# Performance work log

Measured on AMD Instinct MI355X. Metric: run time of the kernel, lower is better.

The kernel has to match this reference:

```python
import math
import jax, jax.numpy as jnp
import numpy as np

SIZE = 8
STEEPNESS = 10.0
BATCH = 262144


def setup_inputs() -> dict:
    key = jax.random.key(0)
    k1, k2 = jax.random.split(key)
    pred_scores = jax.random.normal(k1, (BATCH, SIZE), dtype=jnp.float32)
    labels = jax.random.normal(k2, (BATCH, SIZE), dtype=jnp.float32)
    rank_ema = jnp.zeros((SIZE,), dtype=jnp.float32)  # fresh-module EMA buffer
    return {"pred_scores": pred_scores, "labels": labels, "rank_ema": rank_ema}


def _odd_even_diffsort(x, steepness=STEEPNESS):
    """Differentiable odd-even sorting network (cauchy distribution).
    x: [B, n]. Returns (sorted_values [B, n], perm [B, n, n]) with
    x @ perm == sorted_values (perm tracks columns, matching diffsort)."""
    B, n = x.shape
    P = jnp.broadcast_to(jnp.eye(n, dtype=x.dtype), (B, n, n))
    for layer in range(n):  # odd-even network has n layers for size n
        start = layer % 2
        idx_a = np.arange(start, n - 1, 2)  # static indices
        idx_b = idx_a + 1
        a = x[:, idx_a]
        b = x[:, idx_b]
        # Cauchy CDF of (b - a): alpha -> 1 when pair already sorted (a < b)
        alpha = jnp.arctan(steepness * (b - a)) / math.pi + 0.5  # [B, k]
        new_a = alpha * a + (1.0 - alpha) * b          # soft min -> lower index
        new_b = (1.0 - alpha) * a + alpha * b          # soft max -> upper index
        x = x.at[:, idx_a].set(new_a).at[:, idx_b].set(new_b)
        colA = P[:, :, idx_a]  # [B, n, k]
        colB = P[:, :, idx_b]
        al = alpha[:, None, :]
        P = P.at[:, :, idx_a].set(al * colA + (1.0 - al) * colB)
        P = P.at[:, :, idx_b].set((1.0 - al) * colA + al * colB)
    return x, P


def reference(pred_scores, labels, rank_ema):
    n = pred_scores.shape[-1]
    rank_indices = jnp.argsort(-labels, axis=-1)          # [B, n]
    rank_true = jnp.argsort(rank_indices, axis=-1)        # inverse permutation
    select_rank_ema = rank_ema[rank_true]                 # [B, n]
    shifted = pred_scores - select_rank_ema
    # (EMA buffer update is a detached side effect; it does not affect the loss)
    _, perm_prediction = _odd_even_diffsort(-shifted)
    # one_hot(argsort(-labels)).transpose(-2, -1)
    perm_ground_truth = jnp.swapaxes(jax.nn.one_hot(rank_indices, n, dtype=jnp.float32), -2, -1)
    p = perm_prediction.astype(jnp.float32)
    # torch BCELoss clamps each log term at -100
    log_p = jnp.clip(jnp.log(p), -100.0, None)
    log_1mp = jnp.clip(jnp.log1p(-p), -100.0, None)
    ce_loss = -jnp.mean(perm_ground_truth * log_p + (1.0 - perm_ground_truth) * log_1mp)
    return ce_loss
```

## Files before the change

### kernel.cpp

```cpp
#include <hip/hip_runtime.h>
#include <math.h>

#define BATCH 262144
#define N 8
#define BLK 64
#define NBLK (BATCH / BLK)
#define NCMP 28

typedef float v2f __attribute__((ext_vector_type(2)));

struct Net { int a[NCMP]; unsigned sup2[N / 2][NCMP]; };
constexpr Net make_net() {
    Net n{};
    int k = 0;
    for (int L = 0; L < N; ++L)
        for (int a = (L & 1); a < N - 1; a += 2)
            n.a[k++] = a;
    for (int r = 0; r < N / 2; ++r) {
        unsigned s = (1u << (2 * r)) | (1u << (2 * r + 1));
        for (int q = 0; q < NCMP; ++q) {
            n.sup2[r][q] = s;
            unsigned m = 3u << n.a[q];
            if (s & m) s |= m;
        }
    }
    return n;
}
constexpr Net NET = make_net();

__device__ __forceinline__ float cauchy_alpha(float z10) {
    float az  = __builtin_fabsf(z10);
    bool  big = az > 1.0f;
    float inv = __builtin_amdgcn_rcpf(az);
    float t   = big ? inv : az;
    float t2  = t * t;
    float p   = 0.1417796f;
    p = __builtin_fmaf(p, t2, -0.3258092f);
    p = __builtin_fmaf(p, t2, 0.9992150f);
    float at = p * t;
    float r  = big ? (1.5707963267948966f - at) : at;
    float sr = __builtin_copysignf(r, z10);
    return __builtin_fmaf(sr, 0.31830988618379067f, 0.5f);
}

__global__ __launch_bounds__(BLK, 4) void diffsort_loss_kernel(
    const float* __restrict__ pred,
    const float* __restrict__ labels,
    const float* __restrict__ rank_ema,
    float* __restrict__ partial)
{
    const int row = blockIdx.x * BLK + threadIdx.x;

    __shared__ float ema[N];
    if (threadIdx.x < N) ema[threadIdx.x] = rank_ema[threadIdx.x];
    __syncthreads();

    const float4* lp = (const float4*)(labels + (size_t)row * N);
    const float4* pp = (const float4*)(pred   + (size_t)row * N);
    float4 l0 = lp[0], l1 = lp[1];
    float4 p0 = pp[0], p1 = pp[1];
    float lab[N] = {l0.x, l0.y, l0.z, l0.w, l1.x, l1.y, l1.z, l1.w};
    float prd[N] = {p0.x, p0.y, p0.z, p0.w, p1.x, p1.y, p1.z, p1.w};

    int rt[N];
#pragma unroll
    for (int i = 0; i < N; ++i) rt[i] = 0;
#pragma unroll
    for (int i = 0; i < N; ++i)
#pragma unroll
        for (int j = i + 1; j < N; ++j) {
            unsigned c = lab[j] > lab[i];
            rt[i] += c;
            rt[j] += 1u - c;
        }

    float x[N];
#pragma unroll
    for (int i = 0; i < N; ++i)
        x[i] = ema[rt[i]] - prd[i];

    v2f p2[N / 2][N];
#pragma unroll
    for (int r = 0; r < N / 2; ++r)
#pragma unroll
        for (int j = 0; j < N; ++j) {
            v2f v;
            v.x = (j == 2 * r)     ? 1.0f : 0.0f;
            v.y = (j == 2 * r + 1) ? 1.0f : 0.0f;
            p2[r][j] = v;
        }

#pragma unroll
    for (int k = 0; k < NCMP; ++k) {
        const int ia = NET.a[k], ib = ia + 1;
        const float a = x[ia], b = x[ib];
        const float z = b - a;
        const float alpha = cauchy_alpha(10.0f * z);
        x[ia] = __builtin_fmaf(-alpha, z, b);
        x[ib] = __builtin_fmaf( alpha, z, a);
        v2f al2; al2.x = alpha; al2.y = alpha;
#pragma unroll
        for (int r = 0; r < N / 2; ++r) {
            const bool live = ((NET.sup2[r][k] >> ia) | (NET.sup2[r][k] >> ib)) & 1u;
            if (live) {
                const v2f ca = p2[r][ia], cb = p2[r][ib];
                const v2f d  = ca - cb;
                p2[r][ia] = __builtin_elementwise_fma( al2, d, cb);
                p2[r][ib] = __builtin_elementwise_fma(-al2, d, ca);
            }
        }
    }

    float s = 0.0f;
#pragma unroll
    for (int r = 0; r < N / 2; ++r) {
        const int h0 = rt[2 * r], h1 = rt[2 * r + 1];
        v2f arg; arg.x = 1.0f; arg.y = 1.0f;
#pragma unroll
        for (int j = 0; j < N; ++j) {
            const v2f pv = p2[r][j];
            v2f one; one.x = 1.0f; one.y = 1.0f;
            const v2f qv = one - pv;
            v2f f;
            f.x = (h0 == j) ? pv.x : qv.x;
            f.y = (h1 == j) ? pv.y : qv.y;
            arg *= f;
        }
        s += __logf(fmaxf(arg.x, 1e-37f));
        s += __logf(fmaxf(arg.y, 1e-37f));
    }

#pragma unroll
    for (int off = 32; off > 0; off >>= 1)
        s += __shfl_down(s, off);
    if (threadIdx.x == 0) partial[blockIdx.x] = s;
}

__global__ __launch_bounds__(256) void reduce_partials(
    const float* __restrict__ partial, float* __restrict__ out)
{
    float s = 0.0f;
#pragma unroll
    for (int k = 0; k < NBLK / 256; ++k)
        s += partial[threadIdx.x + k * 256];
#pragma unroll
    for (int off = 32; off > 0; off >>= 1)
        s += __shfl_down(s, off);

    __shared__ float wsum[4];
    const int lane = threadIdx.x & 63;
    const int wid  = threadIdx.x >> 6;
    if (lane == 0) wsum[wid] = s;
    __syncthreads();
    if (threadIdx.x == 0) {
        const float tot = wsum[0] + wsum[1] + wsum[2] + wsum[3];
        out[0] = -tot * (1.0f / 16777216.0f);
    }
}

extern "C" void kernel_launch(void* const* d_in, const int* in_sizes, int n_in,
                              void* d_out, int out_size, void* d_ws, size_t ws_size,
                              hipStream_t stream)
{
    const float* pred     = (const float*)d_in[0];
    const float* labels   = (const float*)d_in[1];
    const float* rank_ema = (const float*)d_in[2];
    float* out     = (float*)d_out;
    float* partial = (float*)d_ws;

    diffsort_loss_kernel<<<NBLK, BLK, 0, stream>>>(pred, labels, rank_ema, partial);
    reduce_partials<<<1, 256, 0, stream>>>(partial, out);
}
```

Baseline: 77.53 us.

## Split each row across two threads, each tracking half the permutation rows

Each batch row is now handled by two threads. Both recompute the label ranks and the sort-value network, and each propagates four of the eight permutation rows, initialised via a lane-dependent select. This doubles thread count and halves per-thread permutation state and register pressure, but duplicates the loads, rank computation and alpha arctan chain. The static liveness pruning of dead permutation entries is removed, so some zero updates are now computed, and the occupancy hint on launch bounds is dropped.

New measurement: 81.65 us. 5.3% more time.

```diff
diff --git a/kernel.cpp b/kernel.cpp
--- a/kernel.cpp
+++ b/kernel.cpp
@@ -4,29 +4,19 @@
 #define BATCH 262144
 #define N 8
 #define BLK 64
-#define NBLK (BATCH / BLK)
+#define ROWS_PER_BLK 32
+#define NBLK (BATCH / ROWS_PER_BLK)
 #define NCMP 28
 
 typedef float v2f __attribute__((ext_vector_type(2)));
 
-struct Net { int a[NCMP]; unsigned sup2[N / 2][NCMP]; };
-constexpr Net make_net() {
-    Net n{};
-    int k = 0;
+constexpr int cmp_a(int k) {
+    int q = 0;
     for (int L = 0; L < N; ++L)
         for (int a = (L & 1); a < N - 1; a += 2)
-            n.a[k++] = a;
-    for (int r = 0; r < N / 2; ++r) {
-        unsigned s = (1u << (2 * r)) | (1u << (2 * r + 1));
-        for (int q = 0; q < NCMP; ++q) {
-            n.sup2[r][q] = s;
-            unsigned m = 3u << n.a[q];
-            if (s & m) s |= m;
-        }
-    }
-    return n;
+            if (q++ == k) return a;
+    return 0;
 }
-constexpr Net NET = make_net();
 
 __device__ __forceinline__ float cauchy_alpha(float z10) {
     float az  = __builtin_fabsf(z10);
@@ -43,16 +33,18 @@
     return __builtin_fmaf(sr, 0.31830988618379067f, 0.5f);
 }
 
-__global__ __launch_bounds__(BLK, 4) void diffsort_loss_kernel(
+__global__ __launch_bounds__(BLK) void diffsort_loss_kernel(
     const float* __restrict__ pred,
     const float* __restrict__ labels,
     const float* __restrict__ rank_ema,
     float* __restrict__ partial)
 {
-    const int row = blockIdx.x * BLK + threadIdx.x;
+    const int tid  = threadIdx.x;
+    const int row  = blockIdx.x * ROWS_PER_BLK + (tid >> 1);
+    const int half = tid & 1;
 
     __shared__ float ema[N];
-    if (threadIdx.x < N) ema[threadIdx.x] = rank_ema[threadIdx.x];
+    if (tid < N) ema[tid] = rank_ema[tid];
     __syncthreads();
 
     const float4* lp = (const float4*)(labels + (size_t)row * N);
@@ -79,20 +71,21 @@
     for (int i = 0; i < N; ++i)
         x[i] = ema[rt[i]] - prd[i];
 
-    v2f p2[N / 2][N];
+    const float h1 = (float)half;
+    const float h0 = 1.0f - h1;
+    v2f p2[2][N];
 #pragma unroll
-    for (int r = 0; r < N / 2; ++r)
+    for (int pr = 0; pr < 2; ++pr)
 #pragma unroll
-        for (int j = 0; j < N; ++j) {
-            v2f v;
-            v.x = (j == 2 * r)     ? 1.0f : 0.0f;
-            v.y = (j == 2 * r + 1) ? 1.0f : 0.0f;
-            p2[r][j] = v;
-        }
+        for (int j = 0; j < N; ++j) { p2[pr][j].x = 0.0f; p2[pr][j].y = 0.0f; }
+    p2[0][0].x = h0; p2[0][4].x = h1;
+    p2[0][1].y = h0; p2[0][5].y = h1;
+    p2[1][2].x = h0; p2[1][6].x = h1;
+    p2[1][3].y = h0; p2[1][7].y = h1;
 
 #pragma unroll
     for (int k = 0; k < NCMP; ++k) {
-        const int ia = NET.a[k], ib = ia + 1;
+        const int ia = cmp_a(k), ib = ia + 1;
         const float a = x[ia], b = x[ib];
         const float z = b - a;
         const float alpha = cauchy_alpha(10.0f * z);
@@ -100,30 +93,27 @@
         x[ib] = __builtin_fmaf( alpha, z, a);
         v2f al2; al2.x = alpha; al2.y = alpha;
 #pragma unroll
-        for (int r = 0; r < N / 2; ++r) {
-            const bool live = ((NET.sup2[r][k] >> ia) | (NET.sup2[r][k] >> ib)) & 1u;
-            if (live) {
-                const v2f ca = p2[r][ia], cb = p2[r][ib];
-                const v2f d  = ca - cb;
-                p2[r][ia] = __builtin_elementwise_fma( al2, d, cb);
-                p2[r][ib] = __builtin_elementwise_fma(-al2, d, ca);
-            }
+        for (int pr = 0; pr < 2; ++pr) {
+            const v2f ca = p2[pr][ia], cb = p2[pr][ib];
+            const v2f d  = ca - cb;
+            p2[pr][ia] = __builtin_elementwise_fma( al2, d, cb);
+            p2[pr][ib] = __builtin_elementwise_fma(-al2, d, ca);
         }
     }
 
+    const int base = 4 * half;
     float s = 0.0f;
 #pragma unroll
-    for (int r = 0; r < N / 2; ++r) {
-        const int h0 = rt[2 * r], h1 = rt[2 * r + 1];
+    for (int pr = 0; pr < 2; ++pr) {
+        const int hx = rt[base + 2 * pr];
+        const int hy = rt[base + 2 * pr + 1];
         v2f arg; arg.x = 1.0f; arg.y = 1.0f;
 #pragma unroll
         for (int j = 0; j < N; ++j) {
-            const v2f pv = p2[r][j];
-            v2f one; one.x = 1.0f; one.y = 1.0f;
-            const v2f qv = one - pv;
+            const v2f pv = p2[pr][j];
             v2f f;
-            f.x = (h0 == j) ? pv.x : qv.x;
-            f.y = (h1 == j) ? pv.y : qv.y;
+            f.x = (hx == j) ? pv.x : (1.0f - pv.x);
+            f.y = (hy == j) ? pv.y : (1.0f - pv.y);
             arg *= f;
         }
         s += __logf(fmaxf(arg.x, 1e-37f));
@@ -133,7 +123,7 @@
 #pragma unroll
     for (int off = 32; off > 0; off >>= 1)
         s += __shfl_down(s, off);
-    if (threadIdx.x == 0) partial[blockIdx.x] = s;
+    if (tid == 0) partial[blockIdx.x] = s;
 }
 
 __global__ __launch_bounds__(256) void reduce_partials(
```

## Fuse final reduction via last-block atomic counter and use packed FP32 inline asm

Applied to the files above, without the earlier changes.

Drops the separate reduce kernel: each block writes its partial sum, bumps an atomic counter, and the last block to finish sums all partials. The counter is cleared with a memset before the launch. The permutation-matrix updates now use v_pk_fma/v_pk_mul/v_pk_add through inline asm. When only one of the two columns is still live, the update is specialised to a single multiply or FMA because the other column is known to be zero. This removes one kernel launch and some ALU work, but adds a memset node, an atomic and threadfences, and the inline asm may limit compiler scheduling.

Result: slower. 209.4 us (+170.0%).

```diff
diff --git a/kernel.cpp b/kernel.cpp
--- a/kernel.cpp
+++ b/kernel.cpp
@@ -8,6 +8,21 @@
 #define NCMP 28
 
 typedef float v2f __attribute__((ext_vector_type(2)));
+
+__device__ __forceinline__ v2f pk_fma(v2f a, v2f b, v2f c) {
+    v2f d; asm("v_pk_fma_f32 %0, %1, %2, %3" : "=v"(d) : "v"(a), "v"(b), "v"(c)); return d;
+}
+__device__ __forceinline__ v2f pk_fma_na(v2f a, v2f b, v2f c) {
+    v2f d; asm("v_pk_fma_f32 %0, %1, %2, %3 neg_lo:[1,0,0] neg_hi:[1,0,0]"
+               : "=v"(d) : "v"(a), "v"(b), "v"(c)); return d;
+}
+__device__ __forceinline__ v2f pk_sub(v2f a, v2f b) {
+    v2f d; asm("v_pk_add_f32 %0, %1, %2 neg_lo:[0,1] neg_hi:[0,1]"
+               : "=v"(d) : "v"(a), "v"(b)); return d;
+}
+__device__ __forceinline__ v2f pk_mul(v2f a, v2f b) {
+    v2f d; asm("v_pk_mul_f32 %0, %1, %2" : "=v"(d) : "v"(a), "v"(b)); return d;
+}
 
 struct Net { int a[NCMP]; unsigned sup2[N / 2][NCMP]; };
 constexpr Net make_net() {
@@ -47,12 +62,15 @@
     const float* __restrict__ pred,
     const float* __restrict__ labels,
     const float* __restrict__ rank_ema,
-    float* __restrict__ partial)
+    float* __restrict__ partial,
+    unsigned int* __restrict__ counter,
+    float* __restrict__ out)
 {
-    const int row = blockIdx.x * BLK + threadIdx.x;
+    const int tid = threadIdx.x;
+    const int row = blockIdx.x * BLK + tid;
 
     __shared__ float ema[N];
-    if (threadIdx.x < N) ema[threadIdx.x] = rank_ema[threadIdx.x];
+    if (tid < N) ema[tid] = rank_ema[tid];
     __syncthreads();
 
     const float4* lp = (const float4*)(labels + (size_t)row * N);
@@ -101,12 +119,21 @@
         v2f al2; al2.x = alpha; al2.y = alpha;
 #pragma unroll
         for (int r = 0; r < N / 2; ++r) {
-            const bool live = ((NET.sup2[r][k] >> ia) | (NET.sup2[r][k] >> ib)) & 1u;
-            if (live) {
+            const bool la = (NET.sup2[r][k] >> ia) & 1u;
+            const bool lb = (NET.sup2[r][k] >> ib) & 1u;
+            if (la && lb) {
                 const v2f ca = p2[r][ia], cb = p2[r][ib];
-                const v2f d  = ca - cb;
-                p2[r][ia] = __builtin_elementwise_fma( al2, d, cb);
-                p2[r][ib] = __builtin_elementwise_fma(-al2, d, ca);
+                const v2f d  = pk_sub(ca, cb);
+                p2[r][ia] = pk_fma(al2, d, cb);
+                p2[r][ib] = pk_fma_na(al2, d, ca);
+            } else if (la) {
+                const v2f ca = p2[r][ia];
+                p2[r][ia] = pk_mul(al2, ca);
+                p2[r][ib] = pk_fma_na(al2, ca, ca);
+            } else if (lb) {
+                const v2f cb = p2[r][ib];
+                p2[r][ia] = pk_fma_na(al2, cb, cb);
+                p2[r][ib] = pk_mul(al2, cb);
             }
         }
     }
@@ -119,12 +146,10 @@
 #pragma unroll
         for (int j = 0; j < N; ++j) {
             const v2f pv = p2[r][j];
-            v2f one; one.x = 1.0f; one.y = 1.0f;
-            const v2f qv = one - pv;
             v2f f;
-            f.x = (h0 == j) ? pv.x : qv.x;
-            f.y = (h1 == j) ? pv.y : qv.y;
-            arg *= f;
+            f.x = (h0 == j) ? pv.x : (1.0f - pv.x);
+            f.y = (h1 == j) ? pv.y : (1.0f - pv.y);
+            arg = pk_mul(arg, f);
         }
         s += __logf(fmaxf(arg.x, 1e-37f));
         s += __logf(fmaxf(arg.y, 1e-37f));
@@ -133,28 +158,24 @@
 #pragma unroll
     for (int off = 32; off > 0; off >>= 1)
         s += __shfl_down(s, off);
-    if (threadIdx.x == 0) partial[blockIdx.x] = s;
-}
+    if (tid == 0) partial[blockIdx.x] = s;
 
-__global__ __launch_bounds__(256) void reduce_partials(
-    const float* __restrict__ partial, float* __restrict__ out)
-{
-    float s = 0.0f;
+    __threadfence();
+    int last = 0;
+    if (tid == 0)
+        last = (atomicAdd(counter, 1u) == (unsigned)(NBLK - 1));
+    last = __shfl(last, 0);
+    if (last) {
+        __threadfence();
+        float t = 0.0f;
 #pragma unroll
-    for (int k = 0; k < NBLK / 256; ++k)
-        s += partial[threadIdx.x + k * 256];
+        for (int k = 0; k < NBLK / BLK; ++k)
+            t += partial[tid + k * BLK];
 #pragma unroll
-    for (int off = 32; off > 0; off >>= 1)
-        s += __shfl_down(s, off);
-
-    __shared__ float wsum[4];
-    const int lane = threadIdx.x & 63;
-    const int wid  = threadIdx.x >> 6;
-    if (lane == 0) wsum[wid] = s;
-    __syncthreads();
-    if (threadIdx.x == 0) {
-        const float tot = wsum[0] + wsum[1] + wsum[2] + wsum[3];
-        out[0] = -tot * (1.0f / 16777216.0f);
+        for (int off = 32; off > 0; off >>= 1)
+            t += __shfl_down(t, off);
+        if (tid == 0)
+            out[0] = -t * (1.0f / 16777216.0f);
     }
 }
 
@@ -165,9 +186,13 @@
     const float* pred     = (const float*)d_in[0];
     const float* labels   = (const float*)d_in[1];
     const float* rank_ema = (const float*)d_in[2];
-    float* out     = (float*)d_out;
-    float* partial = (float*)d_ws;
+    float* out = (float*)d_out;
 
-    diffsort_loss_kernel<<<NBLK, BLK, 0, stream>>>(pred, labels, rank_ema, partial);
-    reduce_partials<<<1, 256, 0, stream>>>(partial, out);
+    float*        partial = (float*)d_ws;
+    unsigned int* counter = (unsigned int*)((char*)d_ws + NBLK * sizeof(float));
+
+    hipMemsetAsync(counter, 0, sizeof(unsigned int), stream);
+
+    diffsort_loss_kernel<<<NBLK, BLK, 0, stream>>>(pred, labels, rank_ema,
+                                                   partial, counter, out);
 }
```
